# Performance work log

Hardware: AMD Instinct MI355X
Metric: run time of the kernel (lower is better)

The kernel has to match this reference:

```python
import jax, jax.numpy as jnp
import numpy as np
from jax.scipy.special import logsumexp

N, D, M = 131072, 32, 256


def setup_inputs() -> dict:
    key = jax.random.key(0)
    k1, k2, k3 = jax.random.split(key, 3)
    X = jax.random.normal(k1, (N, D), dtype=jnp.float32)
    center = jax.random.uniform(k2, (M, D), dtype=jnp.float32)
    # cov_inv_sqrt near identity so det(cov_inv) ~ 1 (fit() would init it via Cholesky);
    # random-matrix init would make det overflow/underflow.
    cov_inv_sqrt = (jnp.eye(D, dtype=jnp.float32)[None, :, :]
                    + 0.02 * jax.random.normal(k3, (M, D, D), dtype=jnp.float32))
    weight = jnp.ones((M,), dtype=jnp.float32)
    threshold = jnp.zeros((1,), dtype=jnp.float32)
    return {"X": X, "center": center, "cov_inv_sqrt": cov_inv_sqrt,
            "weight": weight, "threshold": threshold}


def reference(X, center, cov_inv_sqrt, weight, threshold):
    # refresh(): equal_clusters=True branch
    w = jnp.abs(weight)
    pr = w / w.sum()                                            # [M]
    cov_inv = jnp.einsum('mij,mkj->mik', cov_inv_sqrt, cov_inv_sqrt)  # L L^T, [M,D,D]
    coef = pr * jnp.sqrt(jnp.linalg.det(cov_inv))               # [M]

    # Mahalanobis: q_ij = (x_i - c_j)^T A_j (x_i - c_j), expanded to avoid [N,M,D]:
    #   q_ij = xx_i . A_j_flat - 2 x_i . (A_j c_j) + c_j^T A_j c_j
    n, d = X.shape
    m = center.shape[0]
    A_flat = cov_inv.reshape(m, d * d)                          # [M, D*D]
    xx = (X[:, :, None] * X[:, None, :]).reshape(n, d * d)      # [N, D*D]
    term1 = xx @ A_flat.T                                       # [N, M]
    Ac = jnp.einsum('mkl,ml->mk', cov_inv, center)              # [M, D]
    term2 = X @ Ac.T                                            # [N, M]
    term3 = jnp.einsum('mk,mk->m', center, Ac)                  # [M]
    d_ij = -0.5 * (term1 - 2.0 * term2 + term3[None, :])        # [N, M]

    # weighted logsumexp over clusters: log sum_j coef_j exp(d_ij)
    ll = logsumexp(d_ij, axis=1, b=coef[None, :])               # [N]
    return ll - threshold[0]
```

## Files before the change

kernel.cpp:

```cpp
#include <hip/hip_runtime.h>
#include <hip/hip_bf16.h>
#include <math.h>

#define NPTS 131072
#define DIM 32
#define MCL 256
#define NSTEP 18
#define BPTS 128
#define THREADS 256

typedef __attribute__((ext_vector_type(8))) _Float16 f16x8;
typedef __attribute__((ext_vector_type(2))) _Float16 h2v;
typedef __attribute__((ext_vector_type(2))) unsigned u2v;
typedef __attribute__((ext_vector_type(4))) float f32x4;

__device__ __forceinline__ short f2h(float f) {
    _Float16 h = (_Float16)f;
    union { _Float16 h; short s; } X; X.h = h; return X.s;
}

__global__ __launch_bounds__(256) void gmm_prep(
    const float* __restrict__ center,
    const float* __restrict__ L,
    const float* __restrict__ weight,
    short* __restrict__ G,
    float* __restrict__ cst)
{
    const int m = blockIdx.x;
    const int t = threadIdx.x;
    __shared__ float Ls[DIM][DIM + 1];
    __shared__ float As[DIM][DIM + 1];
    __shared__ float Acs[DIM];
    __shared__ float red[DIM];

    const float* Lm = L + m * DIM * DIM;
    for (int k = t; k < DIM * DIM; k += 256)
        Ls[k >> 5][k & 31] = Lm[k];
    __syncthreads();

    for (int idx = t; idx < DIM * DIM; idx += 256) {
        const int j = idx >> 5, l = idx & 31;
        float a = 0.f;
        #pragma unroll
        for (int d = 0; d < DIM; ++d) a = fmaf(Ls[j][d], Ls[l][d], a);
        As[j][l] = a;
    }
    __syncthreads();

    if (t < DIM) {
        float a = 0.f;
        #pragma unroll
        for (int l = 0; l < DIM; ++l) a = fmaf(As[t][l], center[m * DIM + l], a);
        Acs[t] = a;
        red[t] = a * center[m * DIM + t];
    }
    __syncthreads();

    const int mt = m >> 4, ml = m & 15;
    for (int idx = t; idx < NSTEP * 32; idx += 256) {
        const int s = idx >> 5, k = idx & 31;
        float c;
        if (s == 0)       c = As[k][k] - 1.0f;
        else if (s <= 15) c = 2.0f * As[k][(k + s) & 31];
        else if (s == 16) c = (k < 16) ? 2.0f * As[k][k + 16] : -2.0f * Acs[k - 16];
        else              c = (k < 16) ? -2.0f * Acs[k + 16] : 0.0f;
        G[s * 8192 + mt * 512 + (k >> 3) * 128 + ml * 8 + (k & 7)] = f2h(c);
    }

    if (t < 64) {
        float logdet = 0.f;
        if (t < DIM) {
            float col[DIM];
            #pragma unroll
            for (int r2 = 0; r2 < DIM; ++r2) col[r2] = Ls[r2][t];
            float prodabs = 1.0f;
            #pragma unroll
            for (int k = 0; k < DIM; ++k) {
                const float pv  = __shfl(col[k], k, 64);
                const float rpv = 1.0f / pv;
                const float cjk = col[k];
                #pragma unroll
                for (int t2 = k + 1; t2 < DIM; ++t2) {
                    const float f = __shfl(col[t2], k, 64) * rpv;
                    col[t2] = fmaf(-f, cjk, col[t2]);
                }
                prodabs *= fabsf(pv);
            }
            logdet = logf(prodabs);
        }

        float wsp = 0.f;
        for (int j = t; j < MCL; j += 64) wsp += fabsf(weight[j]);
        #pragma unroll
        for (int d2 = 1; d2 < 64; d2 <<= 1) wsp += __shfl_xor(wsp, d2, 64);

        if (t == 0) {
            float t3 = 0.f;
            #pragma unroll
            for (int j = 0; j < DIM; ++j) t3 += red[j];
            cst[m] = logf(fabsf(weight[m])) - logf(wsp) + logdet - 0.5f * t3;
        }
    }
}

template<int J>
__device__ __forceinline__ unsigned wword(const u2v b0, const u2v b1, const u2v b2) {
    if constexpr (J < 2)      return b0[J];
    else if constexpr (J < 4) return b1[J - 2];
    else                      return b2[J - 4];
}

template<int OFF2, int Q>
__device__ __forceinline__ h2v wpair(const u2v b0, const u2v b1, const u2v b2) {
    constexpr int idx0 = OFF2 + 2 * Q;
    constexpr int wj = idx0 >> 1;
    unsigned u;
    if constexpr ((idx0 & 1) == 0)
        u = wword<wj>(b0, b1, b2);
    else
        u = __builtin_amdgcn_alignbit(wword<wj + 1>(b0, b1, b2),
                                      wword<wj>(b0, b1, b2), 16);
    union { unsigned u; h2v h; } X; X.u = u; return X.h;
}

template<int S, int Q, int OFF2>
__device__ __forceinline__ h2v mkpair(const h2v (&xp)[4], int kg,
                                      const u2v b0, const u2v b1, const u2v b2) {
    if constexpr (S == 0) {
        return xp[Q] * xp[Q];
    } else {
        const h2v wp = wpair<OFF2, Q>(b0, b1, b2);
        if constexpr (S == 16) {
            return (kg < 2) ? (h2v)(xp[Q] * wp) : wp;
        } else if constexpr (S == 17) {
            const h2v z = { (_Float16)0.f, (_Float16)0.f };
            return (kg < 2) ? wp : z;
        } else {
            return xp[Q] * wp;
        }
    }
}

template<int S>
__device__ __forceinline__ void k_step(
    const short* __restrict__ gw,
    const short* __restrict__ Xh,
    const int (&rowh)[4],
    const h2v (&xp)[4][4],
    f16x8 (&bf)[8],
    f32x4 (&acc)[4][8],
    int kg)
{
    constexpr int shv  = (S == 17) ? 16 : S;
    constexpr int off2 = shv & 3;
    const int bq = ((kg * 8 + shv) & 31) & ~3;

    f16x8 af[4];
    #pragma unroll
    for (int i = 0; i < 4; ++i) {
        u2v b0 = {}, b1 = {}, b2 = {};
        if constexpr (S != 0) {
            const short* xr = Xh + rowh[i] + bq;
            b0 = *(const u2v*)(xr);
            b1 = *(const u2v*)(xr + 4);
            if constexpr (off2 != 0) b2 = *(const u2v*)(xr + 8);
        }
        union { f16x8 v; h2v p[4]; } U;
        U.p[0] = mkpair<S, 0, off2>(xp[i], kg, b0, b1, b2);
        U.p[1] = mkpair<S, 1, off2>(xp[i], kg, b0, b1, b2);
        U.p[2] = mkpair<S, 2, off2>(xp[i], kg, b0, b1, b2);
        U.p[3] = mkpair<S, 3, off2>(xp[i], kg, b0, b1, b2);
        af[i] = U.v;
    }

    #pragma unroll
    for (int i = 0; i < 4; ++i)
        #pragma unroll
        for (int j = 0; j < 8; ++j)
            acc[i][j] = __builtin_amdgcn_mfma_f32_16x16x32_f16(
                af[i], bf[j], acc[i][j], 0, 0, 0);

    if constexpr (S + 1 < NSTEP) {
        #pragma unroll
        for (int j = 0; j < 8; ++j)
            bf[j] = *(const f16x8*)(gw + (size_t)(S + 1) * 8192 + j * 512);
    }
    __builtin_amdgcn_sched_barrier(0);
}

template<int S>
__device__ __forceinline__ void k_loop(
    const short* __restrict__ gw, const short* __restrict__ Xh,
    const int (&rowh)[4], const h2v (&xp)[4][4],
    f16x8 (&bf)[8], f32x4 (&acc)[4][8], int kg)
{
    k_step<S>(gw, Xh, rowh, xp, bf, acc, kg);
    if constexpr (S + 1 < NSTEP)
        k_loop<S + 1>(gw, Xh, rowh, xp, bf, acc, kg);
}

__global__ __launch_bounds__(THREADS, 2) void gmm_mfma(
    const float* __restrict__ X,
    const short* __restrict__ G,
    const float* __restrict__ cstw,
    const float* __restrict__ thr,
    float* __restrict__ out)
{
    __shared__ __attribute__((aligned(16))) short Xh[BPTS * 44];
    __shared__ float nrm_s[BPTS];
    __shared__ float cst_s[MCL];
    __shared__ float lse_m[BPTS];
    __shared__ float lse_d[BPTS];

    const int tid  = threadIdx.x;
    const int lane = tid & 63;
    const int w    = tid >> 6;
    const int wr   = w & 1;
    const int wc   = w >> 1;
    const int r    = lane & 15;
    const int kg   = lane >> 4;
    const int P0   = blockIdx.x * BPTS;

    const short* gw = G + wc * 4096 + lane * 8;

    int rowh[4];
    h2v xp[4][4];
    #pragma unroll
    for (int i = 0; i < 4; ++i) {
        const int row = wr * 64 + i * 16 + r;
        rowh[i] = row * 44;
        const float4* xg = reinterpret_cast<const float4*>(
            X + (size_t)(P0 + row) * DIM + kg * 8);
        const float4 a = xg[0], b = xg[1];
        xp[i][0] = h2v{ (_Float16)a.x, (_Float16)a.y };
        xp[i][1] = h2v{ (_Float16)a.z, (_Float16)a.w };
        xp[i][2] = h2v{ (_Float16)b.x, (_Float16)b.y };
        xp[i][3] = h2v{ (_Float16)b.z, (_Float16)b.w };
    }

    {
        const int p = tid >> 1, hf = tid & 1;
        const float4* Xg = reinterpret_cast<const float4*>(
            X + (size_t)(P0 + p) * DIM + hf * 16);
        float part = 0.f;
        #pragma unroll
        for (int q = 0; q < 4; ++q) {
            const float4 v = Xg[q];
            const int kb = hf * 16 + 4 * q;
            Xh[p * 44 + kb + 0] = f2h(v.x);
            Xh[p * 44 + kb + 1] = f2h(v.y);
            Xh[p * 44 + kb + 2] = f2h(v.z);
            Xh[p * 44 + kb + 3] = f2h(v.w);
            if (!hf && q < 2) {
                Xh[p * 44 + 32 + kb + 0] = f2h(v.x);
                Xh[p * 44 + 32 + kb + 1] = f2h(v.y);
                Xh[p * 44 + 32 + kb + 2] = f2h(v.z);
                Xh[p * 44 + 32 + kb + 3] = f2h(v.w);
            }
            part = fmaf(v.x, v.x, part); part = fmaf(v.y, v.y, part);
            part = fmaf(v.z, v.z, part); part = fmaf(v.w, v.w, part);
        }
        part += __shfl_xor(part, 1, 64);
        if (!hf) nrm_s[p] = part;
        cst_s[tid] = cstw[tid];
    }

    f16x8 bf[8];
    #pragma unroll
    for (int j = 0; j < 8; ++j)
        bf[j] = *(const f16x8*)(gw + j * 512);

    __syncthreads();

    f32x4 acc[4][8] = {};
    k_loop<0>(gw, Xh, rowh, xp, bf, acc, kg);

    float cstr[8];
    #pragma unroll
    for (int j = 0; j < 8; ++j)
        cstr[j] = cst_s[wc * 128 + j * 16 + r];

    float mx[16], sm[16];
    #pragma unroll
    for (int i = 0; i < 4; ++i)
        #pragma unroll
        for (int rg = 0; rg < 4; ++rg) {
            const int sl = i * 4 + rg;
            float m_ = -1e30f;
            #pragma unroll
            for (int j = 0; j < 8; ++j)
                m_ = fmaxf(m_, fmaf(acc[i][j][rg], -0.5f, cstr[j]));
            #pragma unroll
            for (int d = 1; d < 16; d <<= 1)
                m_ = fmaxf(m_, __shfl_xor(m_, d, 64));
            float s_ = 0.f;
            #pragma unroll
            for (int j = 0; j < 8; ++j)
                s_ += __expf(fmaf(acc[i][j][rg], -0.5f, cstr[j]) - m_);
            #pragma unroll
            for (int d = 1; d < 16; d <<= 1)
                s_ += __shfl_xor(s_, d, 64);
            mx[sl] = m_; sm[sl] = s_;
        }

    if (wc == 0 && r == 0) {
        #pragma unroll
        for (int i = 0; i < 4; ++i)
            #pragma unroll
            for (int rg = 0; rg < 4; ++rg) {
                const int p2 = wr * 64 + i * 16 + kg * 4 + rg;
                lse_m[p2] = mx[i * 4 + rg];
                lse_d[p2] = sm[i * 4 + rg];
            }
    }
    __syncthreads();
    if (wc == 1 && r == 0) {
        const float thrv = thr[0];
        #pragma unroll
        for (int i = 0; i < 4; ++i)
            #pragma unroll
            for (int rg = 0; rg < 4; ++rg) {
                const int sl = i * 4 + rg;
                const int p2 = wr * 64 + i * 16 + kg * 4 + rg;
                const float om = lse_m[p2], os = lse_d[p2];
                const float nm = fmaxf(mx[sl], om);
                const float ss = sm[sl] * __expf(mx[sl] - nm) + os * __expf(om - nm);
                out[P0 + p2] = nm + __logf(ss) - 0.5f * nrm_s[p2] - thrv;
            }
    }
}

extern "C" void kernel_launch(void* const* d_in, const int* in_sizes, int n_in,
                              void* d_out, int out_size, void* d_ws, size_t ws_size,
                              hipStream_t stream)
{
    const float* X      = (const float*)d_in[0];
    const float* center = (const float*)d_in[1];
    const float* L      = (const float*)d_in[2];
    const float* weight = (const float*)d_in[3];
    const float* thr    = (const float*)d_in[4];
    float* out = (float*)d_out;

    float* cst = (float*)d_ws;
    short* G   = (short*)((char*)d_ws + 1024);

    gmm_prep<<<MCL, 256, 0, stream>>>(center, L, weight, G, cst);
    gmm_mfma<<<NPTS / BPTS, THREADS, 0, stream>>>(X, G, cst, thr, out);
}
```

Measured before the change: 64.02 us.

## Halve block point tile and split clusters across four waves

Each block now handles 64 points instead of 128. The four waves each take a quarter of the 256 clusters instead of a 2x2 split of rows and clusters, which halves per-wave accumulator and B-fragment registers. Occupancy is raised to 3 blocks per SM, and the B-fragment reloads are interleaved with the MFMAs per column. A 4-way logsumexp merge through shared memory replaces the 2-way merge. The trade-off is that each G fragment is now reused over half as many rows, so G traffic per point doubles, and the grid becomes twice as large.

```diff
diff --git a/kernel.cpp b/kernel.cpp
--- a/kernel.cpp
+++ b/kernel.cpp
@@ -6,7 +6,7 @@
 #define DIM 32
 #define MCL 256
 #define NSTEP 18
-#define BPTS 128
+#define BPTS 64
 #define THREADS 256
 
 typedef __attribute__((ext_vector_type(8))) _Float16 f16x8;
@@ -147,8 +147,8 @@
     const short* __restrict__ Xh,
     const int (&rowh)[4],
     const h2v (&xp)[4][4],
-    f16x8 (&bf)[8],
-    f32x4 (&acc)[4][8],
+    f16x8 (&bf)[4],
+    f32x4 (&acc)[4][4],
     int kg)
 {
     constexpr int shv  = (S == 17) ? 16 : S;
@@ -174,15 +174,12 @@
     }
 
     #pragma unroll
-    for (int i = 0; i < 4; ++i)
-        #pragma unroll
-        for (int j = 0; j < 8; ++j)
+    for (int j = 0; j < 4; ++j) {
+        #pragma unroll
+        for (int i = 0; i < 4; ++i)
             acc[i][j] = __builtin_amdgcn_mfma_f32_16x16x32_f16(
                 af[i], bf[j], acc[i][j], 0, 0, 0);
-
-    if constexpr (S + 1 < NSTEP) {
-        #pragma unroll
-        for (int j = 0; j < 8; ++j)
+        if constexpr (S + 1 < NSTEP)
             bf[j] = *(const f16x8*)(gw + (size_t)(S + 1) * 8192 + j * 512);
     }
     __builtin_amdgcn_sched_barrier(0);
@@ -192,14 +189,14 @@
 __device__ __forceinline__ void k_loop(
     const short* __restrict__ gw, const short* __restrict__ Xh,
     const int (&rowh)[4], const h2v (&xp)[4][4],
-    f16x8 (&bf)[8], f32x4 (&acc)[4][8], int kg)
+    f16x8 (&bf)[4], f32x4 (&acc)[4][4], int kg)
 {
     k_step<S>(gw, Xh, rowh, xp, bf, acc, kg);
     if constexpr (S + 1 < NSTEP)
         k_loop<S + 1>(gw, Xh, rowh, xp, bf, acc, kg);
 }
 
-__global__ __launch_bounds__(THREADS, 2) void gmm_mfma(
+__global__ __launch_bounds__(THREADS, 3) void gmm_mfma(
     const float* __restrict__ X,
     const short* __restrict__ G,
     const float* __restrict__ cstw,
@@ -209,25 +206,23 @@
     __shared__ __attribute__((aligned(16))) short Xh[BPTS * 44];
     __shared__ float nrm_s[BPTS];
     __shared__ float cst_s[MCL];
-    __shared__ float lse_m[BPTS];
-    __shared__ float lse_d[BPTS];
+    __shared__ float lse_m[4][BPTS];
+    __shared__ float lse_d[4][BPTS];
 
     const int tid  = threadIdx.x;
     const int lane = tid & 63;
     const int w    = tid >> 6;
-    const int wr   = w & 1;
-    const int wc   = w >> 1;
     const int r    = lane & 15;
     const int kg   = lane >> 4;
     const int P0   = blockIdx.x * BPTS;
 
-    const short* gw = G + wc * 4096 + lane * 8;
+    const short* gw = G + w * 2048 + lane * 8;
 
     int rowh[4];
     h2v xp[4][4];
     #pragma unroll
     for (int i = 0; i < 4; ++i) {
-        const int row = wr * 64 + i * 16 + r;
+        const int row = i * 16 + r;
         rowh[i] = row * 44;
         const float4* xg = reinterpret_cast<const float4*>(
             X + (size_t)(P0 + row) * DIM + kg * 8);
@@ -240,45 +235,47 @@
 
     {
         const int p = tid >> 1, hf = tid & 1;
-        const float4* Xg = reinterpret_cast<const float4*>(
-            X + (size_t)(P0 + p) * DIM + hf * 16);
-        float part = 0.f;
-        #pragma unroll
-        for (int q = 0; q < 4; ++q) {
-            const float4 v = Xg[q];
-            const int kb = hf * 16 + 4 * q;
-            Xh[p * 44 + kb + 0] = f2h(v.x);
-            Xh[p * 44 + kb + 1] = f2h(v.y);
-            Xh[p * 44 + kb + 2] = f2h(v.z);
-            Xh[p * 44 + kb + 3] = f2h(v.w);
-            if (!hf && q < 2) {
-                Xh[p * 44 + 32 + kb + 0] = f2h(v.x);
-                Xh[p * 44 + 32 + kb + 1] = f2h(v.y);
-                Xh[p * 44 + 32 + kb + 2] = f2h(v.z);
-                Xh[p * 44 + 32 + kb + 3] = f2h(v.w);
+        if (tid < 128) {
+            const float4* Xg = reinterpret_cast<const float4*>(
+                X + (size_t)(P0 + p) * DIM + hf * 16);
+            float part = 0.f;
+            #pragma unroll
+            for (int q = 0; q < 4; ++q) {
+                const float4 v = Xg[q];
+                const int kb = hf * 16 + 4 * q;
+                Xh[p * 44 + kb + 0] = f2h(v.x);
+                Xh[p * 44 + kb + 1] = f2h(v.y);
+                Xh[p * 44 + kb + 2] = f2h(v.z);
+                Xh[p * 44 + kb + 3] = f2h(v.w);
+                if (!hf && q < 2) {
+                    Xh[p * 44 + 32 + kb + 0] = f2h(v.x);
+                    Xh[p * 44 + 32 + kb + 1] = f2h(v.y);
+                    Xh[p * 44 + 32 + kb + 2] = f2h(v.z);
+                    Xh[p * 44 + 32 + kb + 3] = f2h(v.w);
+                }
+                part = fmaf(v.x, v.x, part); part = fmaf(v.y, v.y, part);
+                part = fmaf(v.z, v.z, part); part = fmaf(v.w, v.w, part);
             }
-            part = fmaf(v.x, v.x, part); part = fmaf(v.y, v.y, part);
-            part = fmaf(v.z, v.z, part); part = fmaf(v.w, v.w, part);
-        }
-        part += __shfl_xor(part, 1, 64);
-        if (!hf) nrm_s[p] = part;
+            part += __shfl_xor(part, 1, 64);
+            if (!hf) nrm_s[p] = part;
+        }
         cst_s[tid] = cstw[tid];
     }
 
-    f16x8 bf[8];
-    #pragma unroll
-    for (int j = 0; j < 8; ++j)
+    f16x8 bf[4];
+    #pragma unroll
+    for (int j = 0; j < 4; ++j)
         bf[j] = *(const f16x8*)(gw + j * 512);
 
     __syncthreads();
 
-    f32x4 acc[4][8] = {};
+    f32x4 acc[4][4] = {};
     k_loop<0>(gw, Xh, rowh, xp, bf, acc, kg);
 
-    float cstr[8];
-    #pragma unroll
-    for (int j = 0; j < 8; ++j)
-        cstr[j] = cst_s[wc * 128 + j * 16 + r];
+    float cstr[4];
+    #pragma unroll
+    for (int j = 0; j < 4; ++j)
+        cstr[j] = cst_s[w * 64 + j * 16 + r];
 
     float mx[16], sm[16];
     #pragma unroll
@@ -288,14 +285,14 @@
             const int sl = i * 4 + rg;
             float m_ = -1e30f;
             #pragma unroll
-            for (int j = 0; j < 8; ++j)
+            for (int j = 0; j < 4; ++j)
                 m_ = fmaxf(m_, fmaf(acc[i][j][rg], -0.5f, cstr[j]));
             #pragma unroll
             for (int d = 1; d < 16; d <<= 1)
                 m_ = fmaxf(m_, __shfl_xor(m_, d, 64));
             float s_ = 0.f;
             #pragma unroll
-            for (int j = 0; j < 8; ++j)
+            for (int j = 0; j < 4; ++j)
                 s_ += __expf(fmaf(acc[i][j][rg], -0.5f, cstr[j]) - m_);
             #pragma unroll
             for (int d = 1; d < 16; d <<= 1)
@@ -303,30 +300,28 @@
             mx[sl] = m_; sm[sl] = s_;
         }
 
-    if (wc == 0 && r == 0) {
+    if (r == 0) {
         #pragma unroll
         for (int i = 0; i < 4; ++i)
             #pragma unroll
             for (int rg = 0; rg < 4; ++rg) {
-                const int p2 = wr * 64 + i * 16 + kg * 4 + rg;
-                lse_m[p2] = mx[i * 4 + rg];
-                lse_d[p2] = sm[i * 4 + rg];
+                const int p2 = i * 16 + kg * 4 + rg;
+                lse_m[w][p2] = mx[i * 4 + rg];
+                lse_d[w][p2] = sm[i * 4 + rg];
             }
     }
     __syncthreads();
-    if (wc == 1 && r == 0) {
-        const float thrv = thr[0];
-        #pragma unroll
-        for (int i = 0; i < 4; ++i)
-            #pragma unroll
-            for (int rg = 0; rg < 4; ++rg) {
-                const int sl = i * 4 + rg;
-                const int p2 = wr * 64 + i * 16 + kg * 4 + rg;
-                const float om = lse_m[p2], os = lse_d[p2];
-                const float nm = fmaxf(mx[sl], om);
-                const float ss = sm[sl] * __expf(mx[sl] - nm) + os * __expf(om - nm);
-                out[P0 + p2] = nm + __logf(ss) - 0.5f * nrm_s[p2] - thrv;
-            }
+
+    if (tid < BPTS) {
+        float m = lse_m[0][tid], s = lse_d[0][tid];
+        #pragma unroll
+        for (int w2 = 1; w2 < 4; ++w2) {
+            const float pm = lse_m[w2][tid], ps = lse_d[w2][tid];
+            const float nm = fmaxf(m, pm);
+            s = s * __expf(m - nm) + ps * __expf(pm - nm);
+            m = nm;
+        }
+        out[P0 + tid] = m + __logf(s) - 0.5f * nrm_s[tid] - thr[0];
     }
 }
 
```

Measured after the change: 68.06 us. 6.3% more time.
